# Kernel tuning notes

Hardware: AMD Instinct MI355X
Metric: run time of the kernel (lower is better)

Reference implementation:

```python
import jax, jax.numpy as jnp
import numpy as np

N_NODES = 50000
N_EDGES = 800000
N_GRAPHS = 512
DIM = 128


def setup_inputs() -> dict:
    key = jax.random.key(0)
    k1, k2, k3, k4, k5 = jax.random.split(key, 5)
    x = jax.random.normal(k1, (N_NODES, DIM), dtype=jnp.float32)
    edge_index = jax.random.randint(k2, (2, N_EDGES), 0, N_NODES, dtype=jnp.int32)
    batch = jnp.sort(jax.random.randint(k3, (N_NODES,), 0, N_GRAPHS, dtype=jnp.int32))
    scale = 1.0 / np.sqrt(DIM)
    W1 = jax.random.normal(k4, (DIM, DIM), dtype=jnp.float32) * scale
    b1 = jnp.zeros((DIM,), dtype=jnp.float32)
    W2 = jax.random.normal(k5, (DIM, DIM), dtype=jnp.float32) * scale
    b2 = jnp.zeros((DIM,), dtype=jnp.float32)
    return {"x": x, "edge_index": edge_index, "batch": batch,
            "W1": W1, "b1": b1, "W2": W2, "b2": b2}


def reference(x, edge_index, batch, W1, b1, W2, b2):
    n = x.shape[0]
    # GCNConv: add self-loops, symmetric normalization D^-1/2 A D^-1/2
    loop = jnp.arange(n, dtype=edge_index.dtype)
    src = jnp.concatenate([edge_index[0], loop])
    dst = jnp.concatenate([edge_index[1], loop])
    deg = jax.ops.segment_sum(jnp.ones_like(dst, dtype=x.dtype), dst, num_segments=n)
    dinv = jax.lax.rsqrt(jnp.maximum(deg, 1.0))  # deg >= 1 due to self-loops
    norm = (dinv[src] * dinv[dst])[:, None]  # [E+N, 1]

    def gcn(h, W, b):
        h = h @ W                      # [N, D] linear transform
        msg = h[src] * norm            # gather + per-edge scale
        return jax.ops.segment_sum(msg, dst, num_segments=n) + b  # scatter-add

    h = jax.nn.relu(gcn(x, W1, b1))    # dropout is identity in eval mode
    h = gcn(h, W2, b2)

    # global_mean_pool over graph ids
    s = jax.ops.segment_sum(h, batch, num_segments=N_GRAPHS)
    cnt = jax.ops.segment_sum(jnp.ones((n,), dtype=h.dtype), batch, num_segments=N_GRAPHS)
    return s / jnp.maximum(cnt, 1.0)[:, None]
```

## Files before the change

### kernel.cpp

```cpp
#include <hip/hip_runtime.h>

typedef unsigned int uint;
typedef unsigned short ushort_t;
#define DIM 128
#define NCH 256
#define CGRP 32
#define NGRP (NCH / CGRP)

typedef __attribute__((ext_vector_type(8))) short bf16x8;
typedef __attribute__((ext_vector_type(4))) float f32x4;
typedef __attribute__((ext_vector_type(2))) float f32x2;

__device__ inline float bflo(uint u) { return __uint_as_float(u << 16); }
__device__ inline float bfhi(uint u) { return __uint_as_float(u & 0xffff0000u); }
__device__ inline uint packbf2(float a, float b) {
    uint ua = __float_as_uint(a), ub = __float_as_uint(b);
    ua = (ua + 0x7fffu + ((ua >> 16) & 1u)) >> 16;
    ub = (ub + 0x7fffu + ((ub >> 16) & 1u)) & 0xffff0000u;
    return ua | ub;
}

__global__ __launch_bounds__(256) void histprep_kernel(const int* __restrict__ dst,
        uint* __restrict__ part, int nE, int n, int WPC,
        const float* __restrict__ W1, const float* __restrict__ W2,
        uint* __restrict__ Wt1, uint* __restrict__ Wt2,
        float* __restrict__ out, int outQuads, int* __restrict__ done) {
    int b = blockIdx.x;
    if (b >= NCH) {
        int pb = b - NCH;
        if (pb < 64) {
            const float* W = (pb < 32) ? W1 : W2;
            uint* Wt = (pb < 32) ? Wt1 : Wt2;
            int idx = (pb & 31) * 256 + threadIdx.x;
            int c = idx >> 6;
            int kw = idx & 63;
            float a = W[(2 * kw) * DIM + c];
            float bb = W[(2 * kw + 1) * DIM + c];
            Wt[c * 64 + kw] = packbf2(a, bb);
        } else {
            if (pb == 64 && threadIdx.x == 0) *done = 0;
            int q = (pb - 64) * 256 + threadIdx.x;
            if (q < outQuads) ((float4*)out)[q] = make_float4(0.f, 0.f, 0.f, 0.f);
        }
        return;
    }
    extern __shared__ uint h[];
    const int nw4 = (n + 3) >> 2;
    for (int j = threadIdx.x; j < nw4; j += 256) h[j] = 0;
    __syncthreads();
    int chunk = (((nE + NCH - 1) / NCH) + 3) & ~3;
    int lo = b * chunk;
    int hi = min(nE, lo + chunk);
    int hiA = lo + ((hi - lo) & ~3);
    for (int e = lo + threadIdx.x * 4; e < hiA; e += 1024) {
        int4 v = *(const int4*)(dst + e);
        atomicAdd(&h[v.x >> 2], 1u << ((v.x & 3) * 8));
        atomicAdd(&h[v.y >> 2], 1u << ((v.y & 3) * 8));
        atomicAdd(&h[v.z >> 2], 1u << ((v.z & 3) * 8));
        atomicAdd(&h[v.w >> 2], 1u << ((v.w & 3) * 8));
    }
    for (int e = hiA + threadIdx.x; e < hi; e += 256) {
        int d = dst[e];
        atomicAdd(&h[d >> 2], 1u << ((d & 3) * 8));
    }
    __syncthreads();
    uint* pw = part + (size_t)b * WPC;
    for (int j = threadIdx.x; j < nw4; j += 256) pw[j] = h[j];
}

__global__ void reduceA_kernel(uint* __restrict__ part, uint* __restrict__ gsum,
                               int n, int WPC) {
    int j = blockIdx.x * blockDim.x + threadIdx.x;
    int nw4 = (n + 3) >> 2;
    if (j >= nw4) return;
    int g = blockIdx.y;
    int c0 = g * CGRP;
    uint run = 0;
#pragma unroll 8
    for (int c = c0; c < c0 + CGRP; ++c) {
        size_t idx = (size_t)c * WPC + j;
        uint v = part[idx];
        part[idx] = run;
        run += v;
    }
    gsum[(size_t)g * WPC + j] = run;
}

__device__ inline int wave_incl_scan(int v) {
    int lane = threadIdx.x & 63;
#pragma unroll
    for (int off = 1; off < 64; off <<= 1) {
        int u = __shfl_up(v, off, 64);
        if (lane >= off) v += u;
    }
    return v;
}

__global__ __launch_bounds__(256) void gsumscan_kernel(uint* __restrict__ gsum,
        int* __restrict__ deg, int* __restrict__ bsum, int* __restrict__ rowptr,
        int* __restrict__ done, int n, int nb, int WPC) {
    __shared__ int wsum[4];
    __shared__ int lastFlag;
    int t = threadIdx.x;
    int j = blockIdx.x * 256 + t;
    int nw4 = (n + 3) >> 2;
    uint run = 0;
    if (j < nw4) {
#pragma unroll
        for (int g = 0; g < NGRP; ++g) {
            size_t idx = (size_t)g * WPC + j;
            uint v = gsum[idx];
            gsum[idx] = run;
            run += v;
        }
        int base = 4 * j;
        deg[base] = (int)(run & 0xffu);
        if (base + 1 < n) deg[base + 1] = (int)((run >> 8) & 0xffu);
        if (base + 2 < n) deg[base + 2] = (int)((run >> 16) & 0xffu);
        if (base + 3 < n) deg[base + 3] = (int)(run >> 24);
    }
    int s = (int)((run & 0xffu) + ((run >> 8) & 0xffu) + ((run >> 16) & 0xffu) + (run >> 24));
#pragma unroll
    for (int off = 32; off > 0; off >>= 1) s += __shfl_down(s, off, 64);
    if ((t & 63) == 0) wsum[t >> 6] = s;
    __syncthreads();
    if (t == 0) {
        bsum[blockIdx.x] = wsum[0] + wsum[1] + wsum[2] + wsum[3];
        __threadfence();
        int r = atomicAdd(done, 1);
        lastFlag = (r == nb - 1);
    }
    __syncthreads();
    if (lastFlag && t < 64) {
        __threadfence();
        int vv = (t < nb) ? bsum[t] : 0;
        int incl = wave_incl_scan(vv);
        if (t < nb) bsum[t] = incl - vv;
        if (t == 63) rowptr[n] = incl;
    }
}

__global__ void scan3_kernel(const int* __restrict__ deg, const int* __restrict__ bsum,
                             int* __restrict__ rowptr, float* __restrict__ dinv, int n) {
    __shared__ int wsum[16];
    int t = threadIdx.x;
    int i = blockIdx.x * 1024 + t;
    int v = (i < n) ? deg[i] : 0;
    int incl = wave_incl_scan(v);
    int wid = t >> 6;
    if ((t & 63) == 63) wsum[wid] = incl;
    __syncthreads();
    if (t == 0) {
        int run = 0;
#pragma unroll
        for (int w = 0; w < 16; ++w) { int x = wsum[w]; wsum[w] = run; run += x; }
    }
    __syncthreads();
    if (i < n) {
        rowptr[i] = incl - v + wsum[wid] + bsum[blockIdx.x];
        dinv[i] = rsqrtf((float)(v + 1));
    }
}

__global__ __launch_bounds__(256) void fill_kernel(const int* __restrict__ src,
                                                   const int* __restrict__ dst,
                                                   const uint* __restrict__ part,
                                                   const uint* __restrict__ gsum,
                                                   const int* __restrict__ rowptr,
                                                   int* __restrict__ csr,
                                                   int nE, int n, int WPC) {
    extern __shared__ uint cur[];
    const int nw4 = (n + 3) >> 2;
    for (int j = threadIdx.x; j < nw4; j += 256) cur[j] = 0;
    __syncthreads();
    const uint* P = part + (size_t)blockIdx.x * WPC;
    const uint* G = gsum + (size_t)(blockIdx.x / CGRP) * WPC;
    int chunk = (((nE + NCH - 1) / NCH) + 3) & ~3;
    int lo = blockIdx.x * chunk;
    int hi = min(nE, lo + chunk);
    int hiA = lo + ((hi - lo) & ~3);
    for (int e = lo + threadIdx.x * 4; e < hiA; e += 1024) {
        int4 d4 = *(const int4*)(dst + e);
        int4 s4 = *(const int4*)(src + e);
        int dd[4] = {d4.x, d4.y, d4.z, d4.w};
        int ss[4] = {s4.x, s4.y, s4.z, s4.w};
#pragma unroll
        for (int k = 0; k < 4; ++k) {
            int d = dd[k];
            uint sh = (uint)(d & 3) * 8u;
            uint old = atomicAdd(&cur[d >> 2], 1u << sh);
            uint local = (old >> sh) & 0xffu;
            uint pre = ((P[d >> 2] >> sh) & 0xffu) + ((G[d >> 2] >> sh) & 0xffu);
            csr[rowptr[d] + (int)pre + (int)local] = ss[k] << 8;
        }
    }
    for (int e = hiA + threadIdx.x; e < hi; e += 256) {
        int d = dst[e];
        uint sh = (uint)(d & 3) * 8u;
        uint old = atomicAdd(&cur[d >> 2], 1u << sh);
        uint local = (old >> sh) & 0xffu;
        uint pre = ((P[d >> 2] >> sh) & 0xffu) + ((G[d >> 2] >> sh) & 0xffu);
        csr[rowptr[d] + (int)pre + (int)local] = src[e] << 8;
    }
}

template <bool F32IN, bool OUT8>
__global__ __launch_bounds__(256) void gemm_mfma_kernel(const void* __restrict__ Xv,
        const uint* __restrict__ Wt, const float* __restrict__ dinv,
        uint* __restrict__ Hs, int M) {
    __shared__ __align__(16) uint lw[8192];
    __shared__ __align__(16) uint lx[4096];
    const int tid = threadIdx.x;
    const int brow = blockIdx.x * 64;
#pragma unroll
    for (int p = 0; p < 16; ++p) {
        int j = p * 256 + tid;
        int r = j >> 6, kw = j & 63;
        int row = brow + r;
        uint v = 0u;
        if (row < M) {
            if (F32IN) {
                float2 f = ((const float2*)Xv)[(size_t)row * 64 + kw];
                v = packbf2(f.x, f.y);
            } else {
                v = ((const uint*)Xv)[(size_t)row * 64 + kw];
            }
        }
        lx[(r << 6) | (((kw >> 2) ^ (r & 7)) << 2) | (kw & 3)] = v;
    }
#pragma unroll
    for (int p = 0; p < 32; ++p) {
        int j = p * 256 + tid;
        int c = j >> 6, kw = j & 63;
        lw[(c << 6) | (((kw >> 2) ^ (c & 7)) << 2) | (kw & 3)] = Wt[j];
    }
    __syncthreads();
    const int wave = tid >> 6, l = tid & 63;
    const int hl = l >> 4;
    const int arow = (wave << 4) | (l & 15);
    f32x4 acc[8];
#pragma unroll
    for (int f = 0; f < 8; ++f) acc[f] = (f32x4){0.f, 0.f, 0.f, 0.f};
#pragma unroll
    for (int ks = 0; ks < 4; ++ks) {
        int ua = (ks << 2) + hl;
        bf16x8 af = *(const bf16x8*)&lx[(arow << 6) | ((ua ^ (arow & 7)) << 2)];
#pragma unroll
        for (int f = 0; f < 8; ++f) {
            int bcol = (f << 4) | (l & 15);
            bf16x8 bf = *(const bf16x8*)&lw[(bcol << 6) | ((ua ^ (bcol & 7)) << 2)];
            acc[f] = __builtin_amdgcn_mfma_f32_16x16x32_bf16(af, bf, acc[f], 0, 0, 0);
        }
    }
    const int rbase = brow + (wave << 4) + (hl << 2);
    float dv[4];
#pragma unroll
    for (int r = 0; r < 4; ++r) dv[r] = (rbase + r < M) ? dinv[rbase + r] : 0.f;
#pragma unroll
    for (int f = 0; f < 8; ++f) {
#pragma unroll
        for (int r = 0; r < 4; ++r) {
            float mine = acc[f][r] * dv[r];
            float other = __shfl_xor(mine, 1, 64);
            if (!(l & 1)) {
                int row = rbase + r;
                if (row < M) {
                    if (OUT8) {
                        int pk = __builtin_amdgcn_cvt_pk_fp8_f32(mine, other, 0, false);
                        *(ushort_t*)((char*)Hs + (size_t)row * 128 + ((f << 4) | (l & 15))) =
                            (ushort_t)(pk & 0xffff);
                    } else {
                        Hs[(size_t)row * 64 + ((f << 3) | ((l & 15) >> 1))] = packbf2(mine, other);
                    }
                }
            }
        }
    }
}

__device__ inline void g1_acc(uint4 u, float* ax, float* ay) {
    ax[0] += bflo(u.x); ay[0] += bfhi(u.x);
    ax[1] += bflo(u.y); ay[1] += bfhi(u.y);
    ax[2] += bflo(u.z); ay[2] += bfhi(u.z);
    ax[3] += bflo(u.w); ay[3] += bfhi(u.w);
}

__global__ __launch_bounds__(256) void gather1_kernel(const uint* __restrict__ Hs,
        const int* __restrict__ rowptr, const int* __restrict__ csr,
        const float* __restrict__ dinv, const float* __restrict__ b1,
        uint* __restrict__ A, int n) {
    int i = blockIdx.x * 4 + (threadIdx.x >> 6);
    int l = threadIdx.x & 63;
    int slot = l >> 4, q = l & 15;
    if (i >= n) return;
    const char* Hsb = (const char*)Hs;
    const int q16 = q * 16;
    float ax[4] = {0.f, 0.f, 0.f, 0.f}, ay[4] = {0.f, 0.f, 0.f, 0.f};
    if (slot == 0) {
        uint4 u = *(const uint4*)(Hsb + (size_t)i * 256 + q16);
        g1_acc(u, ax, ay);
    }
    int e = rowptr[i], end = rowptr[i + 1];
    for (; e + 16 <= end; e += 16) {
        int o0 = csr[e + slot];
        int o1 = csr[e + 4 + slot];
        int o2 = csr[e + 8 + slot];
        int o3 = csr[e + 12 + slot];
        uint4 u0 = *(const uint4*)(Hsb + (uint)(o0 + q16));
        uint4 u1 = *(const uint4*)(Hsb + (uint)(o1 + q16));
        uint4 u2 = *(const uint4*)(Hsb + (uint)(o2 + q16));
        uint4 u3 = *(const uint4*)(Hsb + (uint)(o3 + q16));
        g1_acc(u0, ax, ay); g1_acc(u1, ax, ay);
        g1_acc(u2, ax, ay); g1_acc(u3, ax, ay);
    }
    for (; e + 4 <= end; e += 4) {
        int o = csr[e + slot];
        uint4 u = *(const uint4*)(Hsb + (uint)(o + q16));
        g1_acc(u, ax, ay);
    }
    int rem = end - e;
    if (slot < rem) {
        int o = csr[e + slot];
        uint4 u = *(const uint4*)(Hsb + (uint)(o + q16));
        g1_acc(u, ax, ay);
    }
#pragma unroll
    for (int k = 0; k < 4; ++k) {
        ax[k] += __shfl_xor(ax[k], 16, 64); ay[k] += __shfl_xor(ay[k], 16, 64);
        ax[k] += __shfl_xor(ax[k], 32, 64); ay[k] += __shfl_xor(ay[k], 32, 64);
    }
    if (slot == 0) {
        float di = dinv[i];
        const float2* bp = (const float2*)(b1 + 8 * q);
        float2 b0 = bp[0], b1v = bp[1], b2v = bp[2], b3v = bp[3];
        uint4 o;
        o.x = packbf2(fmaxf(di * ax[0] + b0.x, 0.f), fmaxf(di * ay[0] + b0.y, 0.f));
        o.y = packbf2(fmaxf(di * ax[1] + b1v.x, 0.f), fmaxf(di * ay[1] + b1v.y, 0.f));
        o.z = packbf2(fmaxf(di * ax[2] + b2v.x, 0.f), fmaxf(di * ay[2] + b2v.y, 0.f));
        o.w = packbf2(fmaxf(di * ax[3] + b3v.x, 0.f), fmaxf(di * ay[3] + b3v.y, 0.f));
        *(uint4*)(A + (size_t)i * 64 + q * 4) = o;
    }
}

__device__ inline void g2_acc(uint2 u, float* ax, float* ay) {
    f32x2 f0 = __builtin_amdgcn_cvt_pk_f32_fp8((int)u.x, false);
    f32x2 f1 = __builtin_amdgcn_cvt_pk_f32_fp8((int)u.x, true);
    f32x2 f2 = __builtin_amdgcn_cvt_pk_f32_fp8((int)u.y, false);
    f32x2 f3 = __builtin_amdgcn_cvt_pk_f32_fp8((int)u.y, true);
    ax[0] += f0.x; ay[0] += f0.y;
    ax[1] += f1.x; ay[1] += f1.y;
    ax[2] += f2.x; ay[2] += f2.y;
    ax[3] += f3.x; ay[3] += f3.y;
}

__global__ __launch_bounds__(512) void gather2_kernel(const char* __restrict__ Hs8,
        const int* __restrict__ rowptr, const int* __restrict__ csr,
        const float* __restrict__ dinv, const int* __restrict__ batch,
        float* __restrict__ out, int n) {
    __shared__ float sh[8][DIM];
    __shared__ int sgid[8];
    int w = threadIdx.x >> 6;
    int l = threadIdx.x & 63;
    int slot = l >> 4, q = l & 15;
    int i = blockIdx.x * 8 + w;
    if (i < n) {
        const int q8 = q * 8;
        float ax[4] = {0.f, 0.f, 0.f, 0.f}, ay[4] = {0.f, 0.f, 0.f, 0.f};
        if (slot == 0) {
            uint2 u = *(const uint2*)(Hs8 + (size_t)i * 128 + q8);
            g2_acc(u, ax, ay);
        }
        int e = rowptr[i], end = rowptr[i + 1];
        for (; e + 16 <= end; e += 16) {
            int o0 = csr[e + slot];
            int o1 = csr[e + 4 + slot];
            int o2 = csr[e + 8 + slot];
            int o3 = csr[e + 12 + slot];
            uint2 u0 = *(const uint2*)(Hs8 + (uint)((o0 >> 1) + q8));
            uint2 u1 = *(const uint2*)(Hs8 + (uint)((o1 >> 1) + q8));
            uint2 u2 = *(const uint2*)(Hs8 + (uint)((o2 >> 1) + q8));
            uint2 u3 = *(const uint2*)(Hs8 + (uint)((o3 >> 1) + q8));
            g2_acc(u0, ax, ay); g2_acc(u1, ax, ay);
            g2_acc(u2, ax, ay); g2_acc(u3, ax, ay);
        }
        for (; e + 4 <= end; e += 4) {
            int o = csr[e + slot];
            uint2 u = *(const uint2*)(Hs8 + (uint)((o >> 1) + q8));
            g2_acc(u, ax, ay);
        }
        int rem = end - e;
        if (slot < rem) {
            int o = csr[e + slot];
            uint2 u = *(const uint2*)(Hs8 + (uint)((o >> 1) + q8));
            g2_acc(u, ax, ay);
        }
#pragma unroll
        for (int k = 0; k < 4; ++k) {
            ax[k] += __shfl_xor(ax[k], 16, 64); ay[k] += __shfl_xor(ay[k], 16, 64);
            ax[k] += __shfl_xor(ax[k], 32, 64); ay[k] += __shfl_xor(ay[k], 32, 64);
        }
        if (slot == 0) {
            float di = dinv[i];
            float* sp = &sh[w][8 * q];
            sp[0] = di * ax[0]; sp[1] = di * ay[0];
            sp[2] = di * ax[1]; sp[3] = di * ay[1];
            sp[4] = di * ax[2]; sp[5] = di * ay[2];
            sp[6] = di * ax[3]; sp[7] = di * ay[3];
            if (q == 0) sgid[w] = batch[i];
        }
    } else if (l == 0) {
        sgid[w] = -1;
    }
    __syncthreads();
    if (threadIdx.x < DIM) {
        int d = threadIdx.x;
        int curg = -1; float run = 0.0f;
#pragma unroll
        for (int r = 0; r < 8; ++r) {
            int g = sgid[r];
            if (g < 0) continue;
            if (g != curg) {
                if (curg >= 0) atomicAdd(&out[(size_t)curg * DIM + d], run);
                curg = g; run = sh[r][d];
            } else {
                run += sh[r][d];
            }
        }
        if (curg >= 0) atomicAdd(&out[(size_t)curg * DIM + d], run);
    }
}

__global__ void fin_kernel(float* __restrict__ out, const int* __restrict__ batch,
                           const float* __restrict__ b2, int n, int nG) {
    int tid = blockIdx.x * blockDim.x + threadIdx.x;
    int g = tid >> 7;
    int d = tid & (DIM - 1);
    if (g >= nG) return;
    int lo = 0, hi = n;
    while (lo < hi) { int m = (lo + hi) >> 1; if (batch[m] < g) lo = m + 1; else hi = m; }
    int s0 = lo;
    hi = n;
    while (lo < hi) { int m = (lo + hi) >> 1; if (batch[m] < g + 1) lo = m + 1; else hi = m; }
    float c = (float)(lo - s0);
    out[tid] = (out[tid] + c * b2[d]) / fmaxf(c, 1.0f);
}

extern "C" void kernel_launch(void* const* d_in, const int* in_sizes, int n_in,
                              void* d_out, int out_size, void* d_ws, size_t ws_size,
                              hipStream_t stream) {
    const float* x     = (const float*)d_in[0];
    const int*   ei    = (const int*)d_in[1];
    const int*   batch = (const int*)d_in[2];
    const float* W1    = (const float*)d_in[3];
    const float* b1    = (const float*)d_in[4];
    const float* W2    = (const float*)d_in[5];
    const float* b2    = (const float*)d_in[6];
    float* out = (float*)d_out;

    const int n  = in_sizes[0] / DIM;
    const int nE = in_sizes[1] / 2;
    const int nG = out_size / DIM;

    const int* src = ei;
    const int* dst = ei + nE;

    const int nw4 = (n + 3) >> 2;
    const int WPC = (nw4 + 3) & ~3;
    const size_t packBytes = (size_t)n * 64 * sizeof(uint);
    const size_t partBytes = (size_t)NCH * WPC * 4;
    const size_t ldsBytes  = (size_t)nw4 * 4;

    char* ws = (char*)d_ws;
    size_t off = 0;
    auto alloc = [&](size_t bytes) { void* p = ws + off; off = (off + bytes + 255) & ~(size_t)255; return p; };
    size_t bigBytes = partBytes > 2 * packBytes ? partBytes : 2 * packBytes;
    char*  big    = (char*)alloc(bigBytes);
    uint*  part   = (uint*)big;
    uint*  Hs     = (uint*)big;
    char*  Hs8    = big;
    uint*  A      = (uint*)(big + packBytes);
    uint*  gsum   = (uint*)alloc((size_t)NGRP * WPC * 4);
    int*   deg    = (int*)alloc((size_t)n * 4);
    int*   done   = (int*)alloc(256);
    float* dinv   = (float*)alloc((size_t)n * 4);
    int*   rowptr = (int*)alloc((size_t)(n + 1) * 4);
    int*   bsum   = (int*)alloc(256);
    uint*  Wt1    = (uint*)alloc(8192 * 4);
    uint*  Wt2    = (uint*)alloc(8192 * 4);
    int*   csr    = (int*)alloc((size_t)nE * 4);

    const int B = 256;
    const int nb = (n + 1023) / 1024;
    const int nwb = (nw4 + B - 1) / B;
    const int outQuads = out_size / 4;

    histprep_kernel<<<NCH + 128, 256, ldsBytes, stream>>>(dst, part, nE, n, WPC,
                                                          W1, W2, Wt1, Wt2, out, outQuads, done);
    reduceA_kernel<<<dim3(nwb, NGRP), B, 0, stream>>>(part, gsum, n, WPC);
    gsumscan_kernel<<<nb, 256, 0, stream>>>(gsum, deg, bsum, rowptr, done, n, nb, WPC);
    scan3_kernel<<<nb, 1024, 0, stream>>>(deg, bsum, rowptr, dinv, n);
    fill_kernel<<<NCH, 256, ldsBytes, stream>>>(src, dst, part, gsum, rowptr, csr, nE, n, WPC);

    gemm_mfma_kernel<true, false><<<(n + 63) / 64, 256, 0, stream>>>(x, Wt1, dinv, Hs, n);
    gather1_kernel<<<(n + 3) / 4, 256, 0, stream>>>(Hs, rowptr, csr, dinv, b1, A, n);

    gemm_mfma_kernel<false, true><<<(n + 63) / 64, 256, 0, stream>>>(A, Wt2, dinv, (uint*)Hs8, n);
    gather2_kernel<<<(n + 7) / 8, 512, 0, stream>>>(Hs8, rowptr, csr, dinv, batch, out, n);

    fin_kernel<<<(nG * DIM + B - 1) / B, B, 0, stream>>>(out, batch, b2, n, nG);
}
```

Baseline: 170.0 us.

## Store layer-1 messages in fp8 and fuse reduceA with gsum scan

New measurement: 214.1 us. +25.9%, slower.

```diff
diff --git a/kernel.cpp b/kernel.cpp
--- a/kernel.cpp
+++ b/kernel.cpp
@@ -11,8 +11,6 @@
 typedef __attribute__((ext_vector_type(4))) float f32x4;
 typedef __attribute__((ext_vector_type(2))) float f32x2;
 
-__device__ inline float bflo(uint u) { return __uint_as_float(u << 16); }
-__device__ inline float bfhi(uint u) { return __uint_as_float(u & 0xffff0000u); }
 __device__ inline uint packbf2(float a, float b) {
     uint ua = __float_as_uint(a), ub = __float_as_uint(b);
     ua = (ua + 0x7fffu + ((ua >> 16) & 1u)) >> 16;
@@ -24,7 +22,8 @@
         uint* __restrict__ part, int nE, int n, int WPC,
         const float* __restrict__ W1, const float* __restrict__ W2,
         uint* __restrict__ Wt1, uint* __restrict__ Wt2,
-        float* __restrict__ out, int outQuads, int* __restrict__ done) {
+        float* __restrict__ out, int outQuads, int* __restrict__ done,
+        int* __restrict__ cntA) {
     int b = blockIdx.x;
     if (b >= NCH) {
         int pb = b - NCH;
@@ -38,7 +37,10 @@
             float bb = W[(2 * kw + 1) * DIM + c];
             Wt[c * 64 + kw] = packbf2(a, bb);
         } else {
-            if (pb == 64 && threadIdx.x == 0) *done = 0;
+            if (pb == 64) {
+                if (threadIdx.x == 0) *done = 0;
+                if (threadIdx.x < 64) cntA[threadIdx.x] = 0;
+            }
             int q = (pb - 64) * 256 + threadIdx.x;
             if (q < outQuads) ((float4*)out)[q] = make_float4(0.f, 0.f, 0.f, 0.f);
         }
@@ -68,24 +70,6 @@
     for (int j = threadIdx.x; j < nw4; j += 256) pw[j] = h[j];
 }
 
-__global__ void reduceA_kernel(uint* __restrict__ part, uint* __restrict__ gsum,
-                               int n, int WPC) {
-    int j = blockIdx.x * blockDim.x + threadIdx.x;
-    int nw4 = (n + 3) >> 2;
-    if (j >= nw4) return;
-    int g = blockIdx.y;
-    int c0 = g * CGRP;
-    uint run = 0;
-#pragma unroll 8
-    for (int c = c0; c < c0 + CGRP; ++c) {
-        size_t idx = (size_t)c * WPC + j;
-        uint v = part[idx];
-        part[idx] = run;
-        run += v;
-    }
-    gsum[(size_t)g * WPC + j] = run;
-}
-
 __device__ inline int wave_incl_scan(int v) {
     int lane = threadIdx.x & 63;
 #pragma unroll
@@ -96,36 +80,59 @@
     return v;
 }
 
-__global__ __launch_bounds__(256) void gsumscan_kernel(uint* __restrict__ gsum,
-        int* __restrict__ deg, int* __restrict__ bsum, int* __restrict__ rowptr,
-        int* __restrict__ done, int n, int nb, int WPC) {
+__global__ __launch_bounds__(256) void reduceAB_kernel(uint* __restrict__ part,
+        uint* __restrict__ gsum, int* __restrict__ deg, int* __restrict__ bsum,
+        int* __restrict__ rowptr, int* __restrict__ cntA, int* __restrict__ done,
+        int n, int nb, int WPC) {
     __shared__ int wsum[4];
     __shared__ int lastFlag;
-    int t = threadIdx.x;
-    int j = blockIdx.x * 256 + t;
-    int nw4 = (n + 3) >> 2;
-    uint run = 0;
+    const int jb = blockIdx.x, g = blockIdx.y;
+    const int t = threadIdx.x;
+    const int j = jb * 256 + t;
+    const int nw4 = (n + 3) >> 2;
     if (j < nw4) {
-#pragma unroll
-        for (int g = 0; g < NGRP; ++g) {
-            size_t idx = (size_t)g * WPC + j;
+        uint run = 0;
+        int c0 = g * CGRP;
+#pragma unroll 8
+        for (int c = c0; c < c0 + CGRP; ++c) {
+            size_t idx = (size_t)c * WPC + j;
+            uint v = part[idx];
+            part[idx] = run;
+            run += v;
+        }
+        gsum[(size_t)g * WPC + j] = run;
+    }
+    __threadfence();
+    __syncthreads();
+    if (t == 0) {
+        int r = atomicAdd(&cntA[jb], 1);
+        lastFlag = (r == NGRP - 1);
+    }
+    __syncthreads();
+    if (!lastFlag) return;
+    __threadfence();
+    uint run2 = 0;
+    if (j < nw4) {
+#pragma unroll
+        for (int gg = 0; gg < NGRP; ++gg) {
+            size_t idx = (size_t)gg * WPC + j;
             uint v = gsum[idx];
-            gsum[idx] = run;
-            run += v;
+            gsum[idx] = run2;
+            run2 += v;
         }
         int base = 4 * j;
-        deg[base] = (int)(run & 0xffu);
-        if (base + 1 < n) deg[base + 1] = (int)((run >> 8) & 0xffu);
-        if (base + 2 < n) deg[base + 2] = (int)((run >> 16) & 0xffu);
-        if (base + 3 < n) deg[base + 3] = (int)(run >> 24);
-    }
-    int s = (int)((run & 0xffu) + ((run >> 8) & 0xffu) + ((run >> 16) & 0xffu) + (run >> 24));
+        deg[base] = (int)(run2 & 0xffu);
+        if (base + 1 < n) deg[base + 1] = (int)((run2 >> 8) & 0xffu);
+        if (base + 2 < n) deg[base + 2] = (int)((run2 >> 16) & 0xffu);
+        if (base + 3 < n) deg[base + 3] = (int)(run2 >> 24);
+    }
+    int s = (int)((run2 & 0xffu) + ((run2 >> 8) & 0xffu) + ((run2 >> 16) & 0xffu) + (run2 >> 24));
 #pragma unroll
     for (int off = 32; off > 0; off >>= 1) s += __shfl_down(s, off, 64);
     if ((t & 63) == 0) wsum[t >> 6] = s;
     __syncthreads();
     if (t == 0) {
-        bsum[blockIdx.x] = wsum[0] + wsum[1] + wsum[2] + wsum[3];
+        bsum[jb] = wsum[0] + wsum[1] + wsum[2] + wsum[3];
         __threadfence();
         int r = atomicAdd(done, 1);
         lastFlag = (r == nb - 1);
@@ -204,10 +211,10 @@
     }
 }
 
-template <bool F32IN, bool OUT8>
+template <bool F32IN>
 __global__ __launch_bounds__(256) void gemm_mfma_kernel(const void* __restrict__ Xv,
         const uint* __restrict__ Wt, const float* __restrict__ dinv,
-        uint* __restrict__ Hs, int M) {
+        char* __restrict__ Hs8, int M) {
     __shared__ __align__(16) uint lw[8192];
     __shared__ __align__(16) uint lx[4096];
     const int tid = threadIdx.x;
@@ -265,27 +272,27 @@
             if (!(l & 1)) {
                 int row = rbase + r;
                 if (row < M) {
-                    if (OUT8) {
-                        int pk = __builtin_amdgcn_cvt_pk_fp8_f32(mine, other, 0, false);
-                        *(ushort_t*)((char*)Hs + (size_t)row * 128 + ((f << 4) | (l & 15))) =
-                            (ushort_t)(pk & 0xffff);
-                    } else {
-                        Hs[(size_t)row * 64 + ((f << 3) | ((l & 15) >> 1))] = packbf2(mine, other);
-                    }
+                    int pk = __builtin_amdgcn_cvt_pk_fp8_f32(mine, other, 0, false);
+                    *(ushort_t*)(Hs8 + (size_t)row * 128 + ((f << 4) | (l & 15))) =
+                        (ushort_t)(pk & 0xffff);
                 }
             }
         }
     }
 }
 
-__device__ inline void g1_acc(uint4 u, float* ax, float* ay) {
-    ax[0] += bflo(u.x); ay[0] += bfhi(u.x);
-    ax[1] += bflo(u.y); ay[1] += bfhi(u.y);
-    ax[2] += bflo(u.z); ay[2] += bfhi(u.z);
-    ax[3] += bflo(u.w); ay[3] += bfhi(u.w);
-}
-
-__global__ __launch_bounds__(256) void gather1_kernel(const uint* __restrict__ Hs,
+__device__ inline void g2_acc(uint2 u, float* ax, float* ay) {
+    f32x2 f0 = __builtin_amdgcn_cvt_pk_f32_fp8((int)u.x, false);
+    f32x2 f1 = __builtin_amdgcn_cvt_pk_f32_fp8((int)u.x, true);
+    f32x2 f2 = __builtin_amdgcn_cvt_pk_f32_fp8((int)u.y, false);
+    f32x2 f3 = __builtin_amdgcn_cvt_pk_f32_fp8((int)u.y, true);
+    ax[0] += f0.x; ay[0] += f0.y;
+    ax[1] += f1.x; ay[1] += f1.y;
+    ax[2] += f2.x; ay[2] += f2.y;
+    ax[3] += f3.x; ay[3] += f3.y;
+}
+
+__global__ __launch_bounds__(256) void gather1_kernel(const char* __restrict__ Hs8,
         const int* __restrict__ rowptr, const int* __restrict__ csr,
         const float* __restrict__ dinv, const float* __restrict__ b1,
         uint* __restrict__ A, int n) {
@@ -293,12 +300,11 @@
     int l = threadIdx.x & 63;
     int slot = l >> 4, q = l & 15;
     if (i >= n) return;
-    const char* Hsb = (const char*)Hs;
-    const int q16 = q * 16;
+    const int q8 = q * 8;
     float ax[4] = {0.f, 0.f, 0.f, 0.f}, ay[4] = {0.f, 0.f, 0.f, 0.f};
     if (slot == 0) {
-        uint4 u = *(const uint4*)(Hsb + (size_t)i * 256 + q16);
-        g1_acc(u, ax, ay);
+        uint2 u = *(const uint2*)(Hs8 + (size_t)i * 128 + q8);
+        g2_acc(u, ax, ay);
     }
     int e = rowptr[i], end = rowptr[i + 1];
     for (; e + 16 <= end; e += 16) {
@@ -306,23 +312,23 @@
         int o1 = csr[e + 4 + slot];
         int o2 = csr[e + 8 + slot];
         int o3 = csr[e + 12 + slot];
-        uint4 u0 = *(const uint4*)(Hsb + (uint)(o0 + q16));
-        uint4 u1 = *(const uint4*)(Hsb + (uint)(o1 + q16));
-        uint4 u2 = *(const uint4*)(Hsb + (uint)(o2 + q16));
-        uint4 u3 = *(const uint4*)(Hsb + (uint)(o3 + q16));
-        g1_acc(u0, ax, ay); g1_acc(u1, ax, ay);
-        g1_acc(u2, ax, ay); g1_acc(u3, ax, ay);
+        uint2 u0 = *(const uint2*)(Hs8 + (uint)((o0 >> 1) + q8));
+        uint2 u1 = *(const uint2*)(Hs8 + (uint)((o1 >> 1) + q8));
+        uint2 u2 = *(const uint2*)(Hs8 + (uint)((o2 >> 1) + q8));
+        uint2 u3 = *(const uint2*)(Hs8 + (uint)((o3 >> 1) + q8));
+        g2_acc(u0, ax, ay); g2_acc(u1, ax, ay);
+        g2_acc(u2, ax, ay); g2_acc(u3, ax, ay);
     }
     for (; e + 4 <= end; e += 4) {
         int o = csr[e + slot];
-        uint4 u = *(const uint4*)(Hsb + (uint)(o + q16));
-        g1_acc(u, ax, ay);
+        uint2 u = *(const uint2*)(Hs8 + (uint)((o >> 1) + q8));
+        g2_acc(u, ax, ay);
     }
     int rem = end - e;
     if (slot < rem) {
         int o = csr[e + slot];
-        uint4 u = *(const uint4*)(Hsb + (uint)(o + q16));
-        g1_acc(u, ax, ay);
+        uint2 u = *(const uint2*)(Hs8 + (uint)((o >> 1) + q8));
+        g2_acc(u, ax, ay);
     }
 #pragma unroll
     for (int k = 0; k < 4; ++k) {
@@ -340,17 +346,6 @@
         o.w = packbf2(fmaxf(di * ax[3] + b3v.x, 0.f), fmaxf(di * ay[3] + b3v.y, 0.f));
         *(uint4*)(A + (size_t)i * 64 + q * 4) = o;
     }
-}
-
-__device__ inline void g2_acc(uint2 u, float* ax, float* ay) {
-    f32x2 f0 = __builtin_amdgcn_cvt_pk_f32_fp8((int)u.x, false);
-    f32x2 f1 = __builtin_amdgcn_cvt_pk_f32_fp8((int)u.x, true);
-    f32x2 f2 = __builtin_amdgcn_cvt_pk_f32_fp8((int)u.y, false);
-    f32x2 f3 = __builtin_amdgcn_cvt_pk_f32_fp8((int)u.y, true);
-    ax[0] += f0.x; ay[0] += f0.y;
-    ax[1] += f1.x; ay[1] += f1.y;
-    ax[2] += f2.x; ay[2] += f2.y;
-    ax[3] += f3.x; ay[3] += f3.y;
 }
 
 __global__ __launch_bounds__(512) void gather2_kernel(const char* __restrict__ Hs8,
@@ -476,12 +471,12 @@
     size_t bigBytes = partBytes > 2 * packBytes ? partBytes : 2 * packBytes;
     char*  big    = (char*)alloc(bigBytes);
     uint*  part   = (uint*)big;
-    uint*  Hs     = (uint*)big;
     char*  Hs8    = big;
     uint*  A      = (uint*)(big + packBytes);
     uint*  gsum   = (uint*)alloc((size_t)NGRP * WPC * 4);
     int*   deg    = (int*)alloc((size_t)n * 4);
     int*   done   = (int*)alloc(256);
+    int*   cntA   = (int*)alloc(256);
     float* dinv   = (float*)alloc((size_t)n * 4);
     int*   rowptr = (int*)alloc((size_t)(n + 1) * 4);
     int*   bsum   = (int*)alloc(256);
@@ -495,16 +490,17 @@
     const int outQuads = out_size / 4;
 
     histprep_kernel<<<NCH + 128, 256, ldsBytes, stream>>>(dst, part, nE, n, WPC,
-                                                          W1, W2, Wt1, Wt2, out, outQuads, done);
-    reduceA_kernel<<<dim3(nwb, NGRP), B, 0, stream>>>(part, gsum, n, WPC);
-    gsumscan_kernel<<<nb, 256, 0, stream>>>(gsum, deg, bsum, rowptr, done, n, nb, WPC);
+                                                          W1, W2, Wt1, Wt2, out, outQuads,
+                                                          done, cntA);
+    reduceAB_kernel<<<dim3(nwb, NGRP), B, 0, stream>>>(part, gsum, deg, bsum, rowptr,
+                                                       cntA, done, n, nb, WPC);
     scan3_kernel<<<nb, 1024, 0, stream>>>(deg, bsum, rowptr, dinv, n);
     fill_kernel<<<NCH, 256, ldsBytes, stream>>>(src, dst, part, gsum, rowptr, csr, nE, n, WPC);
 
-    gemm_mfma_kernel<true, false><<<(n + 63) / 64, 256, 0, stream>>>(x, Wt1, dinv, Hs, n);
-    gather1_kernel<<<(n + 3) / 4, 256, 0, stream>>>(Hs, rowptr, csr, dinv, b1, A, n);
-
-    gemm_mfma_kernel<false, true><<<(n + 63) / 64, 256, 0, stream>>>(A, Wt2, dinv, (uint*)Hs8, n);
+    gemm_mfma_kernel<true><<<(n + 63) / 64, 256, 0, stream>>>(x, Wt1, dinv, Hs8, n);
+    gather1_kernel<<<(n + 3) / 4, 256, 0, stream>>>(Hs8, rowptr, csr, dinv, b1, A, n);
+
+    gemm_mfma_kernel<false><<<(n + 63) / 64, 256, 0, stream>>>(A, Wt2, dinv, Hs8, n);
     gather2_kernel<<<(n + 7) / 8, 512, 0, stream>>>(Hs8, rowptr, csr, dinv, batch, out, n);
 
     fin_kernel<<<(nG * DIM + B - 1) / B, B, 0, stream>>>(out, batch, b2, n, nG);
```
